# Kernel optimization log

Hardware: AMD Instinct MI355X
Metric: run time of the kernel (lower is better)

## Reference

```python
import jax, jax.numpy as jnp
import numpy as np

GRAPH_BIAS_SCALE = 0.8
CTX_GATE_STRENGTH = 2.0
COMMITMENT_COST = 0.25
DECAY = 0.99

N = 262144      # flattened batch*seq tokens
LAT = 128       # latent_dim
DIM = 2 * LAT   # concat(real, imag)
K_SYN = 64
K_SEM = 128


def setup_inputs() -> dict:
    key = jax.random.key(0)
    ks = jax.random.split(key, 18)
    f = jnp.float32
    return {
        "z_fast_re": jax.random.normal(ks[0], (N, LAT), f),
        "z_fast_im": jax.random.normal(ks[1], (N, LAT), f),
        "z_slow_re": jax.random.normal(ks[2], (N, LAT), f),
        "z_slow_im": jax.random.normal(ks[3], (N, LAT), f),
        "cb_syn": jax.random.normal(ks[4], (K_SYN, DIM), f),
        "cb_sem": jax.random.normal(ks[5], (K_SEM, DIM), f),
        "W_syn": jax.random.normal(ks[6], (DIM, K_SYN), f) / np.sqrt(DIM),
        "b_syn": jnp.zeros((K_SYN,), f),
        "W_sem": jax.random.normal(ks[7], (DIM, K_SEM), f) / np.sqrt(DIM),
        "b_sem": jnp.zeros((K_SEM,), f),
        "cl_syn": jnp.zeros((K_SYN,), f),
        "avg_syn": jax.random.normal(ks[8], (K_SYN, DIM), f),
        "cl_sem": jnp.zeros((K_SEM,), f),
        "avg_sem": jax.random.normal(ks[9], (K_SEM, DIM), f),
        "adj_syn": jnp.zeros((K_SYN, K_SYN), f),
        "adj_sem": jnp.zeros((K_SEM, K_SEM), f),
        "prev_syn": jax.random.randint(ks[10], (N,), 0, K_SYN, jnp.int32),
        "prev_sem": jax.random.randint(ks[11], (N,), 0, K_SEM, jnp.int32),
    }


def _vq_step(z_re, z_im, cb, W, b, cl, avg, adj, prev):
    """One context-gated VQ step (training mode). Returns straight-through
    quantized flat latent, loss, indices, and the updated buffers/codebook."""
    K = cb.shape[0]
    zf = jnp.concatenate([z_re, z_im], axis=-1)          # [N, DIM]
    # squared-distance matrix [N, K]
    d = (jnp.sum(zf * zf, axis=1, keepdims=True)
         + jnp.sum(cb * cb, axis=1)
         - 2.0 * zf @ cb.T)
    bias_history = jax.nn.sigmoid(adj[prev])             # [N, K] gather
    bias_context = jax.nn.softmax(zf @ W + b, axis=-1)   # [N, K]
    d = d - (GRAPH_BIAS_SCALE * bias_history + CTX_GATE_STRENGTH * bias_context)
    idx = jnp.argmin(d, axis=1)                          # [N]
    z_q = cb[idx]                                        # [N, DIM] gather
    adj_new = adj.at[prev, idx].set(adj[prev, idx] * 0.995 + 1.0)
    # EMA codebook update (uses detached stats; mutates after z_q already gathered)
    counts = jnp.zeros((K,), zf.dtype).at[idx].add(1.0)          # enc.sum(0)
    embed_sum = jnp.zeros((K, zf.shape[1]), zf.dtype).at[idx].add(zf)  # enc.T @ zf
    cl_new = cl * DECAY + (1.0 - DECAY) * counts
    avg_new = avg * DECAY + (1.0 - DECAY) * embed_sum
    n = jnp.sum(cl_new)
    cs = (cl_new + 1e-6) / (n + K * 1e-6) * n
    cb_new = avg_new / cs[:, None]
    # losses use z_q from the OLD codebook (gathered before the EMA copy)
    sg = jax.lax.stop_gradient
    loss = (jnp.mean((sg(z_q) - zf) ** 2)
            + COMMITMENT_COST * jnp.mean((z_q - sg(zf)) ** 2))
    zq_st = zf + sg(z_q - zf)                            # straight-through
    return zq_st, loss, idx, cl_new, avg_new, cb_new, adj_new


def reference(z_fast_re, z_fast_im, z_slow_re, z_slow_im,
              cb_syn, cb_sem, W_syn, b_syn, W_sem, b_sem,
              cl_syn, avg_syn, cl_sem, avg_sem, adj_syn, adj_sem,
              prev_syn, prev_sem):
    zq_syn, loss_syn, idx_syn, cl_syn_n, avg_syn_n, cb_syn_n, adj_syn_n = _vq_step(
        z_fast_re, z_fast_im, cb_syn, W_syn, b_syn, cl_syn, avg_syn, adj_syn, prev_syn)
    zq_sem, loss_sem, idx_sem, cl_sem_n, avg_sem_n, cb_sem_n, adj_sem_n = _vq_step(
        z_slow_re, z_slow_im, cb_sem, W_sem, b_sem, cl_sem, avg_sem, adj_sem, prev_sem)
    # zq_* are the flat (real||imag) representation of the complex outputs
    return (zq_syn, zq_sem, loss_syn + loss_sem, idx_syn, idx_sem,
            cb_syn_n, cl_syn_n, avg_syn_n, adj_syn_n,
            cb_sem_n, cl_sem_n, avg_sem_n, adj_sem_n)
```

## Files before the change

### kernel.cpp

```cpp
#include <hip/hip_runtime.h>

#define N_TOK 262144
#define LATD  128
#define DIMD  256

using f32x4  = __attribute__((ext_vector_type(4)))  float;
using f32x16 = __attribute__((ext_vector_type(16))) float;
using f16x8  = __attribute__((ext_vector_type(8)))  _Float16;
using f16x2  = __attribute__((ext_vector_type(2)))  _Float16;

#define W_PACK_SYN 0
#define W_PACK_SEM 32768
#define W_CBN_SYN  98304
#define W_CBN_SEM  98368
#define W_IDX_SYN  98496
#define W_IDX_SEM  360640
#define W_CNT_SYN  622784
#define W_CNT_SEM  622848
#define W_EMB_SYN  622976
#define W_EMB_SEM  639360
#define W_MRK_SYN  672128
#define W_MRK_SEM  676224
#define W_LOSSP_SYN 692612
#define W_LOSSP_SEM 700804
#define W_ZERO_BEG 622784
#define W_ZERO_END 692612

#define OFF_ZQ_SYN  0LL
#define OFF_ZQ_SEM  67108864LL
#define OFF_LOSS    134217728LL
#define OFF_IDX_SYN 134217729LL
#define OFF_IDX_SEM 134479873LL
#define OFF_CB_SYN  134742017LL
#define OFF_CL_SYN  134758401LL
#define OFF_AVG_SYN 134758465LL
#define OFF_ADJ_SYN 134774849LL
#define OFF_CB_SEM  134778945LL
#define OFF_CL_SEM  134811713LL
#define OFF_AVG_SEM 134811841LL
#define OFF_ADJ_SEM 134844609LL

__global__ __launch_bounds__(256) void k_init(float* __restrict__ ws) {
  int idx = W_ZERO_BEG + blockIdx.x * 256 + threadIdx.x;
  if (idx < W_ZERO_END) ws[idx] = 0.0f;
}

template <int K>
__global__ __launch_bounds__(256) void k_prep_pack(
    const float* __restrict__ cb, const float* __restrict__ W,
    _Float16* __restrict__ pack) {
  constexpr int R   = 2 * K;
  constexpr int NCT = R / 32;
  constexpr int PER_KT = NCT * 512;
  int t = blockIdx.x * 256 + threadIdx.x;
  int kt = t / PER_KT;
  int r  = t - kt * PER_KT;
  int ct = r >> 9;
  int l  = (r >> 3) & 63;
  int e  = r & 7;
  int j   = kt * 16 + (l >> 5) * 8 + e;
  int col = ct * 32 + (l & 31);
  float x = (col < K) ? cb[col * DIMD + j] : W[j * K + (col - K)];
  _Float16 h = (_Float16)x;
  _Float16 lo = (_Float16)(x - (float)h);
  pack[(size_t)kt * 2 * PER_KT + r]          = h;
  pack[(size_t)kt * 2 * PER_KT + PER_KT + r] = lo;
}

__global__ __launch_bounds__(256) void k_prep_norm(
    const float* __restrict__ cbs, const float* __restrict__ cbm,
    float* __restrict__ ws) {
  __shared__ float red[256];
  int k = blockIdx.x;
  const float* src;
  float* dst;
  if (k < 64) { src = cbs + (size_t)k * DIMD; dst = ws + W_CBN_SYN + k; }
  else        { src = cbm + (size_t)(k - 64) * DIMD; dst = ws + W_CBN_SEM + (k - 64); }
  float v = src[threadIdx.x];
  red[threadIdx.x] = v * v;
  __syncthreads();
  for (int s = 128; s > 0; s >>= 1) {
    if (threadIdx.x < s) red[threadIdx.x] += red[threadIdx.x + s];
    __syncthreads();
  }
  if (threadIdx.x == 0) *dst = red[0];
}

template <int K>
__global__ __launch_bounds__(256, 2) void k_passA(
    const float* __restrict__ zre, const float* __restrict__ zim,
    const _Float16* __restrict__ pack, const float* __restrict__ cbn,
    const float* __restrict__ cb,  const float* __restrict__ bvec,
    const float* __restrict__ adj, const int* __restrict__ prev,
    float* __restrict__ zq_out, float* __restrict__ idxf_out,
    int* __restrict__ idxi_ws, int* __restrict__ mark_ws,
    float* __restrict__ lossp) {
  constexpr int NCT = K / 16;
  constexpr int NH  = K / 32;
  constexpr int PER_KT = NCT * 512;
  __shared__ float wred[4];

  const int tid  = threadIdx.x;
  const int lane = tid & 63;
  const int wv   = tid >> 6;
  const int kg   = lane >> 5;
  const int j    = lane & 31;
  const int t0   = blockIdx.x * 128 + wv * 32;
  const int gt   = t0 + j;

  f32x16 acc[NCT];
#pragma unroll
  for (int t = 0; t < NCT; ++t)
#pragma unroll
    for (int r = 0; r < 16; ++r) acc[t][r] = 0.0f;
  float zn = 0.0f;

  f32x4 v0, v1, nv0, nv1;
  {
    const float* zp = zre + (size_t)gt * LATD + kg * 8;
    v0 = *(const f32x4*)zp;
    v1 = *(const f32x4*)(zp + 4);
  }
#pragma unroll 2
  for (int kt = 0; kt < 16; ++kt) {
    if (kt + 1 < 16) {
      const float* zsrc2 = (kt + 1 < 8) ? zre : zim;
      const float* zp2 = zsrc2 + (size_t)gt * LATD + ((kt + 1) & 7) * 16 + kg * 8;
      nv0 = *(const f32x4*)zp2;
      nv1 = *(const f32x4*)(zp2 + 4);
    }
    f16x8 Bh, Bl;
#pragma unroll
    for (int e = 0; e < 4; ++e) {
      _Float16 h0 = (_Float16)v0[e];
      Bh[e] = h0;       Bl[e] = (_Float16)(v0[e] - (float)h0);
      _Float16 h1 = (_Float16)v1[e];
      Bh[e + 4] = h1;   Bl[e + 4] = (_Float16)(v1[e] - (float)h1);
      zn += v0[e] * v0[e];
      zn += v1[e] * v1[e];
    }
    const _Float16* pk = pack + (size_t)kt * 2 * PER_KT + lane * 8;
#pragma unroll
    for (int t = 0; t < NCT; ++t) {
      f16x8 Ah = *(const f16x8*)(pk + (size_t)t * 512);
      f16x8 Al = *(const f16x8*)(pk + PER_KT + (size_t)t * 512);
      acc[t] = __builtin_amdgcn_mfma_f32_32x32x16_f16(Ah, Bh, acc[t], 0, 0, 0);
      acc[t] = __builtin_amdgcn_mfma_f32_32x32x16_f16(Ah, Bl, acc[t], 0, 0, 0);
      acc[t] = __builtin_amdgcn_mfma_f32_32x32x16_f16(Al, Bh, acc[t], 0, 0, 0);
    }
    v0 = nv0; v1 = nv1;
  }

  const int pv = prev[gt];

  float mx = -1e30f;
#pragma unroll
  for (int t = 0; t < NH; ++t)
#pragma unroll
    for (int q = 0; q < 4; ++q) {
      f32x4 bv4 = *(const f32x4*)&bvec[t * 32 + 8 * q + 4 * kg];
#pragma unroll
      for (int b = 0; b < 4; ++b) {
        acc[NH + t][4 * q + b] += bv4[b];
        mx = fmaxf(mx, acc[NH + t][4 * q + b]);
      }
    }
  mx = fmaxf(mx, __shfl_xor(mx, 32));
  float es = 0.0f;
#pragma unroll
  for (int t = 0; t < NH; ++t)
#pragma unroll
    for (int r = 0; r < 16; ++r) {
      acc[NH + t][r] = __expf(acc[NH + t][r] - mx);
      es += acc[NH + t][r];
    }
  es += __shfl_xor(es, 32);
  const float inv = 1.0f / es;

  const float* adjrow = adj + (size_t)pv * K;
  float best = -1e30f; int bidx = 0; float bdot = 0.0f;
#pragma unroll
  for (int t = 0; t < NH; ++t)
#pragma unroll
    for (int q = 0; q < 4; ++q) {
      const int e0 = t * 32 + 8 * q + 4 * kg;
      f32x4 cb4v = *(const f32x4*)&cbn[e0];
      f32x4 ad4  = *(const f32x4*)&adjrow[e0];
#pragma unroll
      for (int b = 0; b < 4; ++b) {
        int r = 4 * q + b;
        float dot = acc[t][r];
        float sg  = 1.0f / (1.0f + __expf(-ad4[b]));
        float sc  = dot - 0.5f * cb4v[b] + 0.4f * sg + acc[NH + t][r] * inv;
        int   e   = e0 + b;
        if (sc > best || (sc == best && e < bidx)) {
          best = sc; bidx = e; bdot = dot;
        }
      }
    }
  {
    float ob = __shfl_xor(best, 32);
    int   oi = __shfl_xor(bidx, 32);
    float od = __shfl_xor(bdot, 32);
    if (ob > best || (ob == best && oi < bidx)) { best = ob; bidx = oi; bdot = od; }
  }
  const float znf = zn + __shfl_xor(zn, 32);

  float lj = 0.0f;
  if (lane < 32) {
    idxf_out[gt] = (float)bidx;
    idxi_ws[gt]  = bidx;
    mark_ws[pv * K + bidx] = 1;
    lj = cbn[bidx] + znf - 2.0f * bdot;
  }
#pragma unroll
  for (int off = 32; off; off >>= 1) lj += __shfl_xor(lj, off);
  if (lane == 0) wred[wv] = lj;

  const float4* cb4p = (const float4*)cb;
  float4* zq4 = (float4*)zq_out;
#pragma unroll 4
  for (int i = 0; i < 32; ++i) {
    int bi_i = __shfl(bidx, i);
    zq4[(size_t)(t0 + i) * 64 + lane] = cb4p[(size_t)bi_i * 64 + lane];
  }
  __syncthreads();
  if (tid == 0) lossp[blockIdx.x] = wred[0] + wred[1] + wred[2] + wred[3];
}

template <int K>
__global__ __launch_bounds__(256) void k_passB(
    const float* __restrict__ zre, const float* __restrict__ zim,
    const int* __restrict__ idxi,
    float* __restrict__ emb_ws, int* __restrict__ cnt_ws) {
  constexpr int TPB  = 1024;
  constexpr int CH   = 128;
  constexpr int NCT2 = (K == 64) ? 1 : 2;
  __shared__ int idxl[TPB];
  __shared__ int cntl[K];
  __shared__ __align__(16) unsigned short zT[64 * CH];
  const int tid  = threadIdx.x;
  const int lane = tid & 63, wv = tid >> 6;
  const int chunk = blockIdx.x >> 2;
  const int cg    = blockIdx.x & 3;
  const int tbase = chunk * TPB;

  if (tid < K) cntl[tid] = 0;
  __syncthreads();
#pragma unroll
  for (int i = 0; i < TPB / 256; ++i) {
    int id = idxi[tbase + i * 256 + tid];
    idxl[i * 256 + tid] = id;
    if (cg == 0) atomicAdd(&cntl[id], 1);
  }
  __syncthreads();
  if (cg == 0 && tid < K) atomicAdd(&cnt_ws[tid], cntl[tid]);

  const int rt  = (K == 64) ? (wv & 1) : wv;
  const int ct0 = (K == 64) ? (wv >> 1) : 0;
  const int krow = rt * 32 + (lane & 31);
  const int kg   = lane >> 5;
  const float* zsrc = (cg < 2) ? zre : zim;
  const int cbase = (cg & 1) * 64;

  f32x16 acc[NCT2];
#pragma unroll
  for (int c = 0; c < NCT2; ++c)
#pragma unroll
    for (int r = 0; r < 16; ++r) acc[c][r] = 0.0f;

  const int sq = tid & 15;
  const int sp = tid >> 4;

  for (int sc = 0; sc < TPB / CH; ++sc) {
#pragma unroll
    for (int it = 0; it < 4; ++it) {
      int p = sp + it * 16;
      int t = sc * CH + 2 * p;
      const float* zr = zsrc + (size_t)(tbase + t) * LATD + cbase + 4 * sq;
      f32x4 a = *(const f32x4*)zr;
      f32x4 b = *(const f32x4*)(zr + LATD);
#pragma unroll
      for (int c4 = 0; c4 < 4; ++c4) {
        int c = 4 * sq + c4;
        f16x2 pr;
        pr[0] = (_Float16)a[c4];
        pr[1] = (_Float16)b[c4];
        int byte = c * 256 + ((4 * p) ^ ((c & 7) << 4));
        *(f16x2*)((char*)zT + byte) = pr;
      }
    }
    __syncthreads();
#pragma unroll
    for (int st = 0; st < 8; ++st) {
      const int tloc = sc * CH + st * 16 + kg * 8;
      f16x8 Af;
#pragma unroll
      for (int e = 0; e < 8; ++e)
        Af[e] = (idxl[tloc + e] == krow) ? (_Float16)1.0f : (_Float16)0.0f;
#pragma unroll
      for (int c = 0; c < NCT2; ++c) {
        int col = (ct0 + c) * 32 + (lane & 31);
        int byte = col * 256 + (((st * 32 + kg * 16)) ^ ((col & 7) << 4));
        f16x8 Bf = *(const f16x8*)((const char*)zT + byte);
        acc[c] = __builtin_amdgcn_mfma_f32_32x32x16_f16(Af, Bf, acc[c], 0, 0, 0);
      }
    }
    __syncthreads();
  }
#pragma unroll
  for (int c = 0; c < NCT2; ++c)
#pragma unroll
    for (int r = 0; r < 16; ++r) {
      int row = rt * 32 + (r & 3) + 8 * (r >> 2) + 4 * (lane >> 5);
      int col = cg * 64 + (ct0 + c) * 32 + (lane & 31);
      atomicAdd(&emb_ws[row * DIMD + col], acc[c][r]);
    }
}

__global__ __launch_bounds__(256) void k_fin1(
    float* __restrict__ ws, const float* __restrict__ clsi, const float* __restrict__ clmi,
    float* __restrict__ out_cl_syn, float* __restrict__ out_cl_sem, float* __restrict__ out_loss) {
  __shared__ float red[256];
  __shared__ float s1[64], s2[128];
  const int* wsi = (const int*)ws;
  int tid = threadIdx.x;
  float s = 0.0f;
  for (int i = tid; i < 2048; i += 256) s += ws[W_LOSSP_SYN + i];
  for (int i = tid; i < 2048; i += 256) s += ws[W_LOSSP_SEM + i];
  red[tid] = s;
  if (tid < 64) {
    float c  = (float)wsi[W_CNT_SYN + tid];
    float cl = clsi[tid] * 0.99f + 0.01f * c;
    out_cl_syn[tid] = cl; s1[tid] = cl;
  }
  if (tid < 128) {
    float c  = (float)wsi[W_CNT_SEM + tid];
    float cl = clmi[tid] * 0.99f + 0.01f * c;
    out_cl_sem[tid] = cl; s2[tid] = cl;
  }
  __syncthreads();
  for (int st = 128; st > 0; st >>= 1) {
    if (tid < st) red[tid] += red[tid + st];
    __syncthreads();
  }
  if (tid == 0) {
    float n1 = 0.0f; for (int i = 0; i < 64;  ++i) n1 += s1[i];
    float n2 = 0.0f; for (int i = 0; i < 128; ++i) n2 += s2[i];
    ws[W_LOSSP_SYN + 4096] = n1;
    ws[W_LOSSP_SEM + 4096] = n2;
    float denom = (float)N_TOK * 256.0f;
    *out_loss = 1.25f * red[0] / denom;
  }
}

__global__ __launch_bounds__(256) void k_fin2(
    const float* __restrict__ ws,
    const float* __restrict__ avgs, const float* __restrict__ avgm,
    const float* __restrict__ adjs, const float* __restrict__ adjm,
    const float* __restrict__ clsi, const float* __restrict__ clmi,
    float* __restrict__ o_cb_syn, float* __restrict__ o_avg_syn, float* __restrict__ o_adj_syn,
    float* __restrict__ o_cb_sem, float* __restrict__ o_avg_sem, float* __restrict__ o_adj_sem) {
  const int* wsi = (const int*)ws;
  int e = blockIdx.x * 256 + threadIdx.x;
  if (e < 16384) {
    int k = e >> 8;
    float av = avgs[e] * 0.99f + 0.01f * ws[W_EMB_SYN + e];
    o_avg_syn[e] = av;
    float cnt = (float)wsi[W_CNT_SYN + k];
    float cl  = clsi[k] * 0.99f + 0.01f * cnt;
    float n   = ws[W_LOSSP_SYN + 4096];
    float cs  = (cl + 1e-6f) / (n + (float)(64 * 1e-6)) * n;
    o_cb_syn[e] = av / cs;
  } else if (e < 49152) {
    int e2 = e - 16384;
    int k = e2 >> 8;
    float av = avgm[e2] * 0.99f + 0.01f * ws[W_EMB_SEM + e2];
    o_avg_sem[e2] = av;
    float cnt = (float)wsi[W_CNT_SEM + k];
    float cl  = clmi[k] * 0.99f + 0.01f * cnt;
    float n   = ws[W_LOSSP_SEM + 4096];
    float cs  = (cl + 1e-6f) / (n + (float)(128 * 1e-6)) * n;
    o_cb_sem[e2] = av / cs;
  } else if (e < 53248) {
    int a = e - 49152;
    float old = adjs[a];
    o_adj_syn[a] = wsi[W_MRK_SYN + a] ? old * 0.995f + 1.0f : old;
  } else if (e < 69632) {
    int a = e - 53248;
    float old = adjm[a];
    o_adj_sem[a] = wsi[W_MRK_SEM + a] ? old * 0.995f + 1.0f : old;
  }
}

extern "C" void kernel_launch(void* const* d_in, const int* in_sizes, int n_in,
                              void* d_out, int out_size, void* d_ws, size_t ws_size,
                              hipStream_t stream) {
  const float* zfre = (const float*)d_in[0];
  const float* zfim = (const float*)d_in[1];
  const float* zsre = (const float*)d_in[2];
  const float* zsim = (const float*)d_in[3];
  const float* cbs  = (const float*)d_in[4];
  const float* cbm  = (const float*)d_in[5];
  const float* Wsy  = (const float*)d_in[6];
  const float* bsy  = (const float*)d_in[7];
  const float* Wse  = (const float*)d_in[8];
  const float* bse  = (const float*)d_in[9];
  const float* clsi = (const float*)d_in[10];
  const float* avgs = (const float*)d_in[11];
  const float* clmi = (const float*)d_in[12];
  const float* avgm = (const float*)d_in[13];
  const float* adjs = (const float*)d_in[14];
  const float* adjm = (const float*)d_in[15];
  const int*   prvs = (const int*)d_in[16];
  const int*   prvm = (const int*)d_in[17];

  float* out = (float*)d_out;
  float* wsf = (float*)d_ws;
  int*   wsi = (int*)d_ws;
  _Float16* wsh = (_Float16*)d_ws;

  k_init<<<(W_ZERO_END - W_ZERO_BEG + 255) / 256, 256, 0, stream>>>(wsf);
  k_prep_pack<64><<<128, 256, 0, stream>>>(cbs, Wsy, wsh + 2 * W_PACK_SYN);
  k_prep_pack<128><<<256, 256, 0, stream>>>(cbm, Wse, wsh + 2 * W_PACK_SEM);
  k_prep_norm<<<192, 256, 0, stream>>>(cbs, cbm, wsf);

  k_passA<64><<<N_TOK / 128, 256, 0, stream>>>(
      zfre, zfim, wsh + 2 * W_PACK_SYN, wsf + W_CBN_SYN, cbs, bsy, adjs, prvs,
      out + OFF_ZQ_SYN, out + OFF_IDX_SYN, wsi + W_IDX_SYN, wsi + W_MRK_SYN,
      wsf + W_LOSSP_SYN);
  k_passA<128><<<N_TOK / 128, 256, 0, stream>>>(
      zsre, zsim, wsh + 2 * W_PACK_SEM, wsf + W_CBN_SEM, cbm, bse, adjm, prvm,
      out + OFF_ZQ_SEM, out + OFF_IDX_SEM, wsi + W_IDX_SEM, wsi + W_MRK_SEM,
      wsf + W_LOSSP_SEM);

  k_passB<64><<<1024, 256, 0, stream>>>(
      zfre, zfim, wsi + W_IDX_SYN, wsf + W_EMB_SYN, wsi + W_CNT_SYN);
  k_passB<128><<<1024, 256, 0, stream>>>(
      zsre, zsim, wsi + W_IDX_SEM, wsf + W_EMB_SEM, wsi + W_CNT_SEM);

  k_fin1<<<1, 256, 0, stream>>>(wsf, clsi, clmi,
      out + OFF_CL_SYN, out + OFF_CL_SEM, out + OFF_LOSS);
  k_fin2<<<272, 256, 0, stream>>>(wsf, avgs, avgm, adjs, adjm, clsi, clmi,
      out + OFF_CB_SYN, out + OFF_AVG_SYN, out + OFF_ADJ_SYN,
      out + OFF_CB_SEM, out + OFF_AVG_SEM, out + OFF_ADJ_SEM);
}
```

Baseline: 567.4 us.

## Merge launches into fewer kernels and double-buffer the passB staging tile

```diff
diff --git a/kernel.cpp b/kernel.cpp
--- a/kernel.cpp
+++ b/kernel.cpp
@@ -40,24 +40,17 @@
 #define OFF_AVG_SEM 134811841LL
 #define OFF_ADJ_SEM 134844609LL
 
-__global__ __launch_bounds__(256) void k_init(float* __restrict__ ws) {
-  int idx = W_ZERO_BEG + blockIdx.x * 256 + threadIdx.x;
-  if (idx < W_ZERO_END) ws[idx] = 0.0f;
-}
-
 template <int K>
-__global__ __launch_bounds__(256) void k_prep_pack(
-    const float* __restrict__ cb, const float* __restrict__ W,
-    _Float16* __restrict__ pack) {
-  constexpr int R   = 2 * K;
-  constexpr int NCT = R / 32;
+__device__ void prep_pack_body(int bid2, const float* __restrict__ cb,
+                               const float* __restrict__ W, _Float16* __restrict__ pack) {
+  constexpr int NCT = 2 * K / 32;
   constexpr int PER_KT = NCT * 512;
-  int t = blockIdx.x * 256 + threadIdx.x;
+  int t = bid2 * 256 + threadIdx.x;
   int kt = t / PER_KT;
   int r  = t - kt * PER_KT;
-  int ct = r >> 9;
   int l  = (r >> 3) & 63;
   int e  = r & 7;
+  int ct = r >> 9;
   int j   = kt * 16 + (l >> 5) * 8 + e;
   int col = ct * 32 + (l & 31);
   float x = (col < K) ? cb[col * DIMD + j] : W[j * K + (col - K)];
@@ -67,45 +60,53 @@
   pack[(size_t)kt * 2 * PER_KT + PER_KT + r] = lo;
 }
 
-__global__ __launch_bounds__(256) void k_prep_norm(
+__global__ __launch_bounds__(256) void k_prep(
     const float* __restrict__ cbs, const float* __restrict__ cbm,
-    float* __restrict__ ws) {
+    const float* __restrict__ Wsy, const float* __restrict__ Wse,
+    float* __restrict__ ws, _Float16* __restrict__ packs, _Float16* __restrict__ packm) {
   __shared__ float red[256];
-  int k = blockIdx.x;
-  const float* src;
-  float* dst;
-  if (k < 64) { src = cbs + (size_t)k * DIMD; dst = ws + W_CBN_SYN + k; }
-  else        { src = cbm + (size_t)(k - 64) * DIMD; dst = ws + W_CBN_SEM + (k - 64); }
-  float v = src[threadIdx.x];
-  red[threadIdx.x] = v * v;
-  __syncthreads();
-  for (int s = 128; s > 0; s >>= 1) {
-    if (threadIdx.x < s) red[threadIdx.x] += red[threadIdx.x + s];
+  const int bid = blockIdx.x, tid = threadIdx.x;
+  if (bid < 273) {
+    int idx = W_ZERO_BEG + bid * 256 + tid;
+    if (idx < W_ZERO_END) ws[idx] = 0.0f;
+  } else if (bid < 401) {
+    prep_pack_body<64>(bid - 273, cbs, Wsy, packs);
+  } else if (bid < 657) {
+    prep_pack_body<128>(bid - 401, cbm, Wse, packm);
+  } else {
+    int k = bid - 657;
+    const float* src; float* dst;
+    if (k < 64) { src = cbs + (size_t)k * DIMD; dst = ws + W_CBN_SYN + k; }
+    else        { src = cbm + (size_t)(k - 64) * DIMD; dst = ws + W_CBN_SEM + (k - 64); }
+    float v = src[tid];
+    red[tid] = v * v;
     __syncthreads();
-  }
-  if (threadIdx.x == 0) *dst = red[0];
+    for (int s = 128; s > 0; s >>= 1) {
+      if (tid < s) red[tid] += red[tid + s];
+      __syncthreads();
+    }
+    if (tid == 0) *dst = red[0];
+  }
 }
 
 template <int K>
-__global__ __launch_bounds__(256, 2) void k_passA(
+__device__ void passA_body(int bid,
     const float* __restrict__ zre, const float* __restrict__ zim,
     const _Float16* __restrict__ pack, const float* __restrict__ cbn,
     const float* __restrict__ cb,  const float* __restrict__ bvec,
     const float* __restrict__ adj, const int* __restrict__ prev,
     float* __restrict__ zq_out, float* __restrict__ idxf_out,
     int* __restrict__ idxi_ws, int* __restrict__ mark_ws,
-    float* __restrict__ lossp) {
+    float* __restrict__ lossp, float* wred) {
   constexpr int NCT = K / 16;
   constexpr int NH  = K / 32;
   constexpr int PER_KT = NCT * 512;
-  __shared__ float wred[4];
-
   const int tid  = threadIdx.x;
   const int lane = tid & 63;
   const int wv   = tid >> 6;
   const int kg   = lane >> 5;
   const int j    = lane & 31;
-  const int t0   = blockIdx.x * 128 + wv * 32;
+  const int t0   = bid * 128 + wv * 32;
   const int gt   = t0 + j;
 
   f32x16 acc[NCT];
@@ -225,24 +226,46 @@
     zq4[(size_t)(t0 + i) * 64 + lane] = cb4p[(size_t)bi_i * 64 + lane];
   }
   __syncthreads();
-  if (tid == 0) lossp[blockIdx.x] = wred[0] + wred[1] + wred[2] + wred[3];
+  if (tid == 0) lossp[bid] = wred[0] + wred[1] + wred[2] + wred[3];
+}
+
+__global__ __launch_bounds__(256, 2) void k_passA_all(
+    const float* __restrict__ zfre, const float* __restrict__ zfim,
+    const float* __restrict__ zsre, const float* __restrict__ zsim,
+    const _Float16* __restrict__ packs, const _Float16* __restrict__ packm,
+    const float* __restrict__ cbns, const float* __restrict__ cbnm,
+    const float* __restrict__ cbs, const float* __restrict__ cbm,
+    const float* __restrict__ bsy, const float* __restrict__ bse,
+    const float* __restrict__ adjs, const float* __restrict__ adjm,
+    const int* __restrict__ prvs, const int* __restrict__ prvm,
+    float* __restrict__ zqs, float* __restrict__ zqm,
+    float* __restrict__ idxfs, float* __restrict__ idxfm,
+    int* __restrict__ idxis, int* __restrict__ idxim,
+    int* __restrict__ mrks, int* __restrict__ mrkm,
+    float* __restrict__ lossps, float* __restrict__ losspm) {
+  __shared__ float wred[4];
+  const int bid = blockIdx.x >> 1;
+  if ((blockIdx.x & 1) == 0)
+    passA_body<64>(bid, zfre, zfim, packs, cbns, cbs, bsy, adjs, prvs,
+                   zqs, idxfs, idxis, mrks, lossps, wred);
+  else
+    passA_body<128>(bid, zsre, zsim, packm, cbnm, cbm, bse, adjm, prvm,
+                    zqm, idxfm, idxim, mrkm, losspm, wred);
 }
 
 template <int K>
-__global__ __launch_bounds__(256) void k_passB(
+__device__ void passB_body(int fid,
     const float* __restrict__ zre, const float* __restrict__ zim,
     const int* __restrict__ idxi,
-    float* __restrict__ emb_ws, int* __restrict__ cnt_ws) {
-  constexpr int TPB  = 1024;
+    float* __restrict__ emb_ws, int* __restrict__ cnt_ws,
+    int* idxl, int* cntl, unsigned short* zT) {
+  constexpr int TPB  = 2048;
   constexpr int CH   = 128;
   constexpr int NCT2 = (K == 64) ? 1 : 2;
-  __shared__ int idxl[TPB];
-  __shared__ int cntl[K];
-  __shared__ __align__(16) unsigned short zT[64 * CH];
   const int tid  = threadIdx.x;
   const int lane = tid & 63, wv = tid >> 6;
-  const int chunk = blockIdx.x >> 2;
-  const int cg    = blockIdx.x & 3;
+  const int cg    = fid & 3;
+  const int chunk = fid >> 2;
   const int tbase = chunk * TPB;
 
   if (tid < K) cntl[tid] = 0;
@@ -272,7 +295,8 @@
   const int sq = tid & 15;
   const int sp = tid >> 4;
 
-  for (int sc = 0; sc < TPB / CH; ++sc) {
+  auto stage = [&](int sc) {
+    unsigned short* zb = zT + (sc & 1) * 8192;
 #pragma unroll
     for (int it = 0; it < 4; ++it) {
       int p = sp + it * 16;
@@ -287,10 +311,16 @@
         pr[0] = (_Float16)a[c4];
         pr[1] = (_Float16)b[c4];
         int byte = c * 256 + ((4 * p) ^ ((c & 7) << 4));
-        *(f16x2*)((char*)zT + byte) = pr;
+        *(f16x2*)((char*)zb + byte) = pr;
       }
     }
+  };
+
+  stage(0);
+  for (int sc = 0; sc < TPB / CH; ++sc) {
     __syncthreads();
+    if (sc + 1 < TPB / CH) stage(sc + 1);
+    const unsigned short* zb = zT + (sc & 1) * 8192;
 #pragma unroll
     for (int st = 0; st < 8; ++st) {
       const int tloc = sc * CH + st * 16 + kg * 8;
@@ -301,12 +331,11 @@
 #pragma unroll
       for (int c = 0; c < NCT2; ++c) {
         int col = (ct0 + c) * 32 + (lane & 31);
-        int byte = col * 256 + (((st * 32 + kg * 16)) ^ ((col & 7) << 4));
-        f16x8 Bf = *(const f16x8*)((const char*)zT + byte);
+        int byte = col * 256 + ((st * 32 + kg * 16) ^ ((col & 7) << 4));
+        f16x8 Bf = *(const f16x8*)((const char*)zb + byte);
         acc[c] = __builtin_amdgcn_mfma_f32_32x32x16_f16(Af, Bf, acc[c], 0, 0, 0);
       }
     }
-    __syncthreads();
   }
 #pragma unroll
   for (int c = 0; c < NCT2; ++c)
@@ -318,58 +347,73 @@
     }
 }
 
-__global__ __launch_bounds__(256) void k_fin1(
-    float* __restrict__ ws, const float* __restrict__ clsi, const float* __restrict__ clmi,
-    float* __restrict__ out_cl_syn, float* __restrict__ out_cl_sem, float* __restrict__ out_loss) {
-  __shared__ float red[256];
-  __shared__ float s1[64], s2[128];
-  const int* wsi = (const int*)ws;
-  int tid = threadIdx.x;
-  float s = 0.0f;
-  for (int i = tid; i < 2048; i += 256) s += ws[W_LOSSP_SYN + i];
-  for (int i = tid; i < 2048; i += 256) s += ws[W_LOSSP_SEM + i];
-  red[tid] = s;
-  if (tid < 64) {
-    float c  = (float)wsi[W_CNT_SYN + tid];
-    float cl = clsi[tid] * 0.99f + 0.01f * c;
-    out_cl_syn[tid] = cl; s1[tid] = cl;
-  }
-  if (tid < 128) {
-    float c  = (float)wsi[W_CNT_SEM + tid];
-    float cl = clmi[tid] * 0.99f + 0.01f * c;
-    out_cl_sem[tid] = cl; s2[tid] = cl;
-  }
-  __syncthreads();
-  for (int st = 128; st > 0; st >>= 1) {
-    if (tid < st) red[tid] += red[tid + st];
-    __syncthreads();
-  }
-  if (tid == 0) {
-    float n1 = 0.0f; for (int i = 0; i < 64;  ++i) n1 += s1[i];
-    float n2 = 0.0f; for (int i = 0; i < 128; ++i) n2 += s2[i];
-    ws[W_LOSSP_SYN + 4096] = n1;
-    ws[W_LOSSP_SEM + 4096] = n2;
-    float denom = (float)N_TOK * 256.0f;
-    *out_loss = 1.25f * red[0] / denom;
-  }
-}
-
-__global__ __launch_bounds__(256) void k_fin2(
-    const float* __restrict__ ws,
+__global__ __launch_bounds__(256) void k_passB_all(
+    const float* __restrict__ zfre, const float* __restrict__ zfim,
+    const float* __restrict__ zsre, const float* __restrict__ zsim,
+    const int* __restrict__ idxis, const int* __restrict__ idxim,
+    float* __restrict__ embs, float* __restrict__ embm,
+    int* __restrict__ cnts, int* __restrict__ cntm) {
+  __shared__ int idxl[2048];
+  __shared__ int cntl[128];
+  __shared__ __align__(16) unsigned short zT[2 * 8192];
+  const int fid = blockIdx.x >> 1;
+  if ((blockIdx.x & 1) == 0)
+    passB_body<64>(fid, zfre, zfim, idxis, embs, cnts, idxl, cntl, zT);
+  else
+    passB_body<128>(fid, zsre, zsim, idxim, embm, cntm, idxl, cntl, zT);
+}
+
+__global__ __launch_bounds__(256) void k_fin(
+    const float* __restrict__ ws, const float* __restrict__ clsi, const float* __restrict__ clmi,
     const float* __restrict__ avgs, const float* __restrict__ avgm,
     const float* __restrict__ adjs, const float* __restrict__ adjm,
-    const float* __restrict__ clsi, const float* __restrict__ clmi,
+    float* __restrict__ o_loss, float* __restrict__ o_cl_syn, float* __restrict__ o_cl_sem,
     float* __restrict__ o_cb_syn, float* __restrict__ o_avg_syn, float* __restrict__ o_adj_syn,
     float* __restrict__ o_cb_sem, float* __restrict__ o_avg_sem, float* __restrict__ o_adj_sem) {
+  __shared__ float sred[256];
   const int* wsi = (const int*)ws;
-  int e = blockIdx.x * 256 + threadIdx.x;
+  const int bid = blockIdx.x, tid = threadIdx.x;
+  if (bid == 0) {
+    float s = 0.0f;
+    for (int i = tid; i < 2048; i += 256) s += ws[W_LOSSP_SYN + i];
+    for (int i = tid; i < 2048; i += 256) s += ws[W_LOSSP_SEM + i];
+    sred[tid] = s;
+    __syncthreads();
+    for (int st = 128; st > 0; st >>= 1) {
+      if (tid < st) sred[tid] += sred[tid + st];
+      __syncthreads();
+    }
+    if (tid < 64)
+      o_cl_syn[tid] = clsi[tid] * 0.99f + 0.01f * (float)wsi[W_CNT_SYN + tid];
+    if (tid < 128)
+      o_cl_sem[tid] = clmi[tid] * 0.99f + 0.01f * (float)wsi[W_CNT_SEM + tid];
+    if (tid == 0)
+      *o_loss = 1.25f * sred[0] / ((float)N_TOK * 256.0f);
+    return;
+  }
+  const int e = (bid - 1) * 256 + tid;
+  float n = 0.0f;
+  if (e < 49152) {
+    const bool syn = e < 16384;
+    const int KK = syn ? 64 : 128;
+    const float* clp = syn ? clsi : clmi;
+    const int cntoff = syn ? W_CNT_SYN : W_CNT_SEM;
+    float v = 0.0f;
+    if (tid < KK) v = clp[tid] * 0.99f + 0.01f * (float)wsi[cntoff + tid];
+    sred[tid] = v;
+    __syncthreads();
+    for (int st = 128; st > 0; st >>= 1) {
+      if (tid < st) sred[tid] += sred[tid + st];
+      __syncthreads();
+    }
+    n = sred[0];
+  }
   if (e < 16384) {
     int k = e >> 8;
     float av = avgs[e] * 0.99f + 0.01f * ws[W_EMB_SYN + e];
     o_avg_syn[e] = av;
     float cnt = (float)wsi[W_CNT_SYN + k];
     float cl  = clsi[k] * 0.99f + 0.01f * cnt;
-    float n   = ws[W_LOSSP_SYN + 4096];
     float cs  = (cl + 1e-6f) / (n + (float)(64 * 1e-6)) * n;
     o_cb_syn[e] = av / cs;
   } else if (e < 49152) {
@@ -379,7 +423,6 @@
     o_avg_sem[e2] = av;
     float cnt = (float)wsi[W_CNT_SEM + k];
     float cl  = clmi[k] * 0.99f + 0.01f * cnt;
-    float n   = ws[W_LOSSP_SEM + 4096];
     float cs  = (cl + 1e-6f) / (n + (float)(128 * 1e-6)) * n;
     o_cb_sem[e2] = av / cs;
   } else if (e < 53248) {
@@ -420,28 +463,28 @@
   int*   wsi = (int*)d_ws;
   _Float16* wsh = (_Float16*)d_ws;
 
-  k_init<<<(W_ZERO_END - W_ZERO_BEG + 255) / 256, 256, 0, stream>>>(wsf);
-  k_prep_pack<64><<<128, 256, 0, stream>>>(cbs, Wsy, wsh + 2 * W_PACK_SYN);
-  k_prep_pack<128><<<256, 256, 0, stream>>>(cbm, Wse, wsh + 2 * W_PACK_SEM);
-  k_prep_norm<<<192, 256, 0, stream>>>(cbs, cbm, wsf);
-
-  k_passA<64><<<N_TOK / 128, 256, 0, stream>>>(
-      zfre, zfim, wsh + 2 * W_PACK_SYN, wsf + W_CBN_SYN, cbs, bsy, adjs, prvs,
-      out + OFF_ZQ_SYN, out + OFF_IDX_SYN, wsi + W_IDX_SYN, wsi + W_MRK_SYN,
-      wsf + W_LOSSP_SYN);
-  k_passA<128><<<N_TOK / 128, 256, 0, stream>>>(
-      zsre, zsim, wsh + 2 * W_PACK_SEM, wsf + W_CBN_SEM, cbm, bse, adjm, prvm,
-      out + OFF_ZQ_SEM, out + OFF_IDX_SEM, wsi + W_IDX_SEM, wsi + W_MRK_SEM,
-      wsf + W_LOSSP_SEM);
-
-  k_passB<64><<<1024, 256, 0, stream>>>(
-      zfre, zfim, wsi + W_IDX_SYN, wsf + W_EMB_SYN, wsi + W_CNT_SYN);
-  k_passB<128><<<1024, 256, 0, stream>>>(
-      zsre, zsim, wsi + W_IDX_SEM, wsf + W_EMB_SEM, wsi + W_CNT_SEM);
-
-  k_fin1<<<1, 256, 0, stream>>>(wsf, clsi, clmi,
-      out + OFF_CL_SYN, out + OFF_CL_SEM, out + OFF_LOSS);
-  k_fin2<<<272, 256, 0, stream>>>(wsf, avgs, avgm, adjs, adjm, clsi, clmi,
+  k_prep<<<849, 256, 0, stream>>>(cbs, cbm, Wsy, Wse, wsf,
+      wsh + 2 * W_PACK_SYN, wsh + 2 * W_PACK_SEM);
+
+  k_passA_all<<<4096, 256, 0, stream>>>(
+      zfre, zfim, zsre, zsim,
+      wsh + 2 * W_PACK_SYN, wsh + 2 * W_PACK_SEM,
+      wsf + W_CBN_SYN, wsf + W_CBN_SEM,
+      cbs, cbm, bsy, bse, adjs, adjm, prvs, prvm,
+      out + OFF_ZQ_SYN, out + OFF_ZQ_SEM,
+      out + OFF_IDX_SYN, out + OFF_IDX_SEM,
+      wsi + W_IDX_SYN, wsi + W_IDX_SEM,
+      wsi + W_MRK_SYN, wsi + W_MRK_SEM,
+      wsf + W_LOSSP_SYN, wsf + W_LOSSP_SEM);
+
+  k_passB_all<<<1024, 256, 0, stream>>>(
+      zfre, zfim, zsre, zsim,
+      wsi + W_IDX_SYN, wsi + W_IDX_SEM,
+      wsf + W_EMB_SYN, wsf + W_EMB_SEM,
+      wsi + W_CNT_SYN, wsi + W_CNT_SEM);
+
+  k_fin<<<273, 256, 0, stream>>>(wsf, clsi, clmi, avgs, avgm, adjs, adjm,
+      out + OFF_LOSS, out + OFF_CL_SYN, out + OFF_CL_SEM,
       out + OFF_CB_SYN, out + OFF_AVG_SYN, out + OFF_ADJ_SYN,
       out + OFF_CB_SEM, out + OFF_AVG_SEM, out + OFF_ADJ_SEM);
 }
```

Measured after the change: 613.2 us. 8.1% more time.
